# Kernel optimization log

Measured on AMD Instinct MI355X. Metric: run time of the kernel, lower is better.

## Reference

```python
import jax, jax.numpy as jnp
import numpy as np

L = 10.0
N_UP = 2048
N_DN = 2048
N = N_UP + N_DN
HIDDEN = 32


def _neural_decayed(x, w1, b1, wo, bo):
    # x: (M,) pair distances. Tiny MLP 1 -> HIDDEN -> 1 with compact-support decay.
    x_cut = L / 2
    xn = jnp.clip(x / x_cut, 0.0, 1.0 - 1e-05)
    decay = jnp.exp(1.0 - 1.0 / (1.0 - xn ** 2))
    h = jax.nn.swish(decay[:, None] @ w1 + b1)      # (M, HIDDEN)
    out = (h @ wo + bo).ravel()                      # (M,)
    return out * decay


def setup_inputs() -> dict:
    key = jax.random.key(0)
    ks = jax.random.split(key, 9)
    rs = jax.random.uniform(ks[0], (N, 3), dtype=jnp.float32) * L
    s = 1.0 / np.sqrt(HIDDEN)
    return {
        "rs": rs,
        "same_w1": jax.random.normal(ks[1], (1, HIDDEN), jnp.float32),
        "same_b1": jnp.zeros((HIDDEN,), jnp.float32),
        "same_wo": jax.random.normal(ks[2], (HIDDEN, 1), jnp.float32) * s,
        "same_bo": jnp.zeros((1,), jnp.float32),
        "diff_w1": jax.random.normal(ks[3], (1, HIDDEN), jnp.float32),
        "diff_b1": jnp.zeros((HIDDEN,), jnp.float32),
        "diff_wo": jax.random.normal(ks[4], (HIDDEN, 1), jnp.float32) * s,
        "diff_bo": jnp.zeros((1,), jnp.float32),
    }


def reference(rs, same_w1, same_b1, same_wo, same_bo, diff_w1, diff_b1, diff_wo, diff_bo):
    # Pairwise minimum-image displacements: (N, N, 3)
    disps = rs[:, None, :] - rs[None, :, :]
    disps = (disps + L / 2) % L - L / 2
    mask = ~jnp.eye(N, dtype=bool)
    disps = jnp.where(mask[:, :, None], disps, 0.0)
    r_ij = jnp.sqrt(jnp.sum(disps ** 2, axis=-1) + 1e-15)  # (N, N)

    up_up = r_ij[:N_UP, :N_UP]
    dn_dn = r_ij[N_UP:, N_UP:]
    up_dn = r_ij[N_UP:, :N_UP]

    f_uu = _neural_decayed(up_up.ravel(), same_w1, same_b1, same_wo, same_bo).reshape(up_up.shape)
    f_dd = _neural_decayed(dn_dn.ravel(), same_w1, same_b1, same_wo, same_bo).reshape(dn_dn.shape)
    f_ud = _neural_decayed(up_dn.ravel(), diff_w1, diff_b1, diff_wo, diff_bo).reshape(up_dn.shape)

    forces = jnp.zeros((N, N), jnp.float32)
    forces = forces.at[:N_UP, :N_UP].set(f_uu)
    forces = forces.at[N_UP:, N_UP:].set(f_dd)
    forces = forces.at[N_UP:, :N_UP].set(f_ud)
    forces = forces.at[:N_UP, N_UP:].set(f_ud.T)
    forces = jnp.where(mask, forces, 0.0)

    backflow = jnp.sum(forces[:, :, None] * disps, axis=1)  # (N, 3)
    return rs + backflow
```

## Files before the change

kernel.cpp:

```cpp
#include <hip/hip_runtime.h>
#include <math.h>

#define N_TOT 4096
#define N_UPC 2048
#define HID 32
#define M_LUT 2048
#define ITILE 256
#define JCH 128

__device__ float2 g_lut[2 * M_LUT];

__device__ __forceinline__ float eval_F(float s, const float* __restrict__ w1,
                                        const float* __restrict__ b1,
                                        const float* __restrict__ wo, float bo) {
  float r = sqrtf(s + 1e-15f);
  float xn = fminf(r * 0.2f, 1.0f - 1e-5f);
  float dcy = __expf(1.0f - 1.0f / (1.0f - xn * xn));
  float acc = bo;
#pragma unroll
  for (int k = 0; k < HID; ++k) {
    float z = fmaf(dcy, w1[k], b1[k]);
    float h = z / (1.0f + __expf(-z));
    acc = fmaf(h, wo[k], acc);
  }
  return acc * dcy;
}

__global__ void lut_init_kernel(const float* __restrict__ rs,
    const float* __restrict__ sw1, const float* __restrict__ sb1,
    const float* __restrict__ swo, const float* __restrict__ sbo,
    const float* __restrict__ dw1, const float* __restrict__ db1,
    const float* __restrict__ dwo, const float* __restrict__ dbo,
    float* __restrict__ out) {
  const float DSF = 25.0f / (float)(M_LUT - 1);
  int t = blockIdx.x * blockDim.x + threadIdx.x;
  if (t < 2 * M_LUT) {
    int tab = t >> 11;
    int m = t & (M_LUT - 1);
    const float* w1 = tab ? dw1 : sw1;
    const float* b1 = tab ? db1 : sb1;
    const float* wo = tab ? dwo : swo;
    float bo = tab ? dbo[0] : sbo[0];
    float s0 = m * DSF;
    float f0 = eval_F(s0, w1, b1, wo, bo);
    float f1 = eval_F(s0 + DSF, w1, b1, wo, bo);
    g_lut[t] = make_float2(f0, f1 - f0);
  }
  if (t < 3 * N_TOT) out[t] = rs[t];
}

__global__ __launch_bounds__(256) void pair_kernel(const float* __restrict__ rs,
                                                   float* __restrict__ out) {
  __shared__ float2 lut[M_LUT];

  int itile = blockIdx.x & 15;
  int jc = blockIdx.x >> 4;
  const bool same_spin = ((jc < (N_UPC / JCH)) == (itile < 8));
  const float2* __restrict__ src = g_lut + (same_spin ? 0 : M_LUT);
  for (int t = threadIdx.x; t < M_LUT; t += ITILE) lut[t] = src[t];

  int i = itile * ITILE + threadIdx.x;
  float xi = rs[3 * i + 0];
  float yi = rs[3 * i + 1];
  float zi = rs[3 * i + 2];
  __syncthreads();

  const float INV_DS = (float)(M_LUT - 1) / 25.0f;

  float ax = 0.f, ay = 0.f, az = 0.f;
  int j0 = jc * JCH;
#pragma unroll 8
  for (int jj = 0; jj < JCH; ++jj) {
    int j = j0 + jj;
    float dx = xi - rs[3 * j + 0];
    float dy = yi - rs[3 * j + 1];
    float dz = zi - rs[3 * j + 2];
    dx = fmaf(-10.0f, rintf(dx * 0.1f), dx);
    dy = fmaf(-10.0f, rintf(dy * 0.1f), dy);
    dz = fmaf(-10.0f, rintf(dz * 0.1f), dz);
    float s = fmaf(dx, dx, fmaf(dy, dy, dz * dz));
    float u = s * INV_DS;
    int idx = min((int)u, M_LUT - 2);
    float w = u - (float)idx;
    float2 e = lut[idx];
    float F = fmaf(w, e.y, e.x);
    ax = fmaf(F, dx, ax);
    ay = fmaf(F, dy, ay);
    az = fmaf(F, dz, az);
  }
  atomicAdd(&out[3 * i + 0], ax);
  atomicAdd(&out[3 * i + 1], ay);
  atomicAdd(&out[3 * i + 2], az);
}

extern "C" void kernel_launch(void* const* d_in, const int* in_sizes, int n_in,
                              void* d_out, int out_size, void* d_ws, size_t ws_size,
                              hipStream_t stream) {
  const float* rs = (const float*)d_in[0];
  lut_init_kernel<<<64, 256, 0, stream>>>(
      rs,
      (const float*)d_in[1], (const float*)d_in[2], (const float*)d_in[3],
      (const float*)d_in[4],
      (const float*)d_in[5], (const float*)d_in[6], (const float*)d_in[7],
      (const float*)d_in[8],
      (float*)d_out);
  pair_kernel<<<(N_TOT / ITILE) * (N_TOT / JCH), ITILE, 0, stream>>>(
      rs, (float*)d_out);
}
```

Measured before the change: 91.00 us.

## Assign one row per 32 lanes and reduce with shuffles instead of atomics

The pair loop is reorganised so each group of 32 lanes owns one particle row i and strides over all 4096 j, covering both spin tables loaded together into LDS. Partial sums are combined with xor shuffles and written directly with rs added in, which removes the global atomics and the initial copy of rs into the output. Each block now loads both LUTs (32 KB of LDS), and lanes read rs[j] at strided addresses instead of broadcast addresses, which may cost more memory traffic. The grid becomes 512 blocks doing 4096 pairs per row.

```diff
diff --git a/kernel.cpp b/kernel.cpp
--- a/kernel.cpp
+++ b/kernel.cpp
@@ -5,8 +5,8 @@
 #define N_UPC 2048
 #define HID 32
 #define M_LUT 2048
-#define ITILE 256
-#define JCH 128
+#define ROWS_PER_BLK 8
+#define LANES_PER_ROW 32
 
 __device__ float2 g_lut[2 * M_LUT];
 
@@ -26,12 +26,11 @@
   return acc * dcy;
 }
 
-__global__ void lut_init_kernel(const float* __restrict__ rs,
+__global__ void lut_init_kernel(
     const float* __restrict__ sw1, const float* __restrict__ sb1,
     const float* __restrict__ swo, const float* __restrict__ sbo,
     const float* __restrict__ dw1, const float* __restrict__ db1,
-    const float* __restrict__ dwo, const float* __restrict__ dbo,
-    float* __restrict__ out) {
+    const float* __restrict__ dwo, const float* __restrict__ dbo) {
   const float DSF = 25.0f / (float)(M_LUT - 1);
   int t = blockIdx.x * blockDim.x + threadIdx.x;
   if (t < 2 * M_LUT) {
@@ -46,64 +45,78 @@
     float f1 = eval_F(s0 + DSF, w1, b1, wo, bo);
     g_lut[t] = make_float2(f0, f1 - f0);
   }
-  if (t < 3 * N_TOT) out[t] = rs[t];
 }
 
 __global__ __launch_bounds__(256) void pair_kernel(const float* __restrict__ rs,
                                                    float* __restrict__ out) {
-  __shared__ float2 lut[M_LUT];
+  __shared__ float2 lut[2 * M_LUT];
+  {
+    const float4* __restrict__ src = (const float4*)g_lut;
+    float4* dst = (float4*)lut;
+    for (int t = threadIdx.x; t < M_LUT; t += 256) dst[t] = src[t];
+  }
 
-  int itile = blockIdx.x & 15;
-  int jc = blockIdx.x >> 4;
-  const bool same_spin = ((jc < (N_UPC / JCH)) == (itile < 8));
-  const float2* __restrict__ src = g_lut + (same_spin ? 0 : M_LUT);
-  for (int t = threadIdx.x; t < M_LUT; t += ITILE) lut[t] = src[t];
-
-  int i = itile * ITILE + threadIdx.x;
-  float xi = rs[3 * i + 0];
-  float yi = rs[3 * i + 1];
-  float zi = rs[3 * i + 2];
+  const int row_local = threadIdx.x >> 5;
+  const int lane = threadIdx.x & 31;
+  const int i = blockIdx.x * ROWS_PER_BLK + row_local;
+  const float xi = rs[3 * i + 0];
+  const float yi = rs[3 * i + 1];
+  const float zi = rs[3 * i + 2];
   __syncthreads();
 
+  const bool i_up = (i < N_UPC);
+  const float2* __restrict__ tabA = lut + (i_up ? 0 : M_LUT);
+  const float2* __restrict__ tabB = lut + (i_up ? M_LUT : 0);
   const float INV_DS = (float)(M_LUT - 1) / 25.0f;
 
   float ax = 0.f, ay = 0.f, az = 0.f;
-  int j0 = jc * JCH;
+
+#pragma unroll 2
+  for (int half = 0; half < 2; ++half) {
+    const float2* __restrict__ tab = half ? tabB : tabA;
+    int jbase = half * N_UPC + lane;
 #pragma unroll 8
-  for (int jj = 0; jj < JCH; ++jj) {
-    int j = j0 + jj;
-    float dx = xi - rs[3 * j + 0];
-    float dy = yi - rs[3 * j + 1];
-    float dz = zi - rs[3 * j + 2];
-    dx = fmaf(-10.0f, rintf(dx * 0.1f), dx);
-    dy = fmaf(-10.0f, rintf(dy * 0.1f), dy);
-    dz = fmaf(-10.0f, rintf(dz * 0.1f), dz);
-    float s = fmaf(dx, dx, fmaf(dy, dy, dz * dz));
-    float u = s * INV_DS;
-    int idx = min((int)u, M_LUT - 2);
-    float w = u - (float)idx;
-    float2 e = lut[idx];
-    float F = fmaf(w, e.y, e.x);
-    ax = fmaf(F, dx, ax);
-    ay = fmaf(F, dy, ay);
-    az = fmaf(F, dz, az);
+    for (int jj = 0; jj < N_UPC / LANES_PER_ROW; ++jj) {
+      int j = jbase + jj * LANES_PER_ROW;
+      float dx = xi - rs[3 * j + 0];
+      float dy = yi - rs[3 * j + 1];
+      float dz = zi - rs[3 * j + 2];
+      dx = fmaf(-10.0f, rintf(dx * 0.1f), dx);
+      dy = fmaf(-10.0f, rintf(dy * 0.1f), dy);
+      dz = fmaf(-10.0f, rintf(dz * 0.1f), dz);
+      float s = fmaf(dx, dx, fmaf(dy, dy, dz * dz));
+      float u = s * INV_DS;
+      int idx = min((int)u, M_LUT - 2);
+      float w = u - (float)idx;
+      float2 e = tab[idx];
+      float F = fmaf(w, e.y, e.x);
+      ax = fmaf(F, dx, ax);
+      ay = fmaf(F, dy, ay);
+      az = fmaf(F, dz, az);
+    }
   }
-  atomicAdd(&out[3 * i + 0], ax);
-  atomicAdd(&out[3 * i + 1], ay);
-  atomicAdd(&out[3 * i + 2], az);
+
+#pragma unroll
+  for (int m = 16; m >= 1; m >>= 1) {
+    ax += __shfl_xor(ax, m, 32);
+    ay += __shfl_xor(ay, m, 32);
+    az += __shfl_xor(az, m, 32);
+  }
+  if (lane == 0) {
+    out[3 * i + 0] = xi + ax;
+    out[3 * i + 1] = yi + ay;
+    out[3 * i + 2] = zi + az;
+  }
 }
 
 extern "C" void kernel_launch(void* const* d_in, const int* in_sizes, int n_in,
                               void* d_out, int out_size, void* d_ws, size_t ws_size,
                               hipStream_t stream) {
   const float* rs = (const float*)d_in[0];
-  lut_init_kernel<<<64, 256, 0, stream>>>(
-      rs,
+  lut_init_kernel<<<16, 256, 0, stream>>>(
       (const float*)d_in[1], (const float*)d_in[2], (const float*)d_in[3],
       (const float*)d_in[4],
       (const float*)d_in[5], (const float*)d_in[6], (const float*)d_in[7],
-      (const float*)d_in[8],
-      (float*)d_out);
-  pair_kernel<<<(N_TOT / ITILE) * (N_TOT / JCH), ITILE, 0, stream>>>(
-      rs, (float*)d_out);
+      (const float*)d_in[8]);
+  pair_kernel<<<N_TOT / ROWS_PER_BLK, 256, 0, stream>>>(rs, (float*)d_out);
 }
```

Measured after the change: 86.76 us. -4.7%, faster.
